# Performance work log

Hardware: AMD Instinct MI355X
Metric: run time of the kernel (lower is better)

Reference implementation:

```python
import jax, jax.numpy as jnp
import numpy as np

NUM_USERS = 100_000
NUM_JOBS = 100_000
N_NODES = NUM_USERS + NUM_JOBS
E = 3_200_000
D = 64  # embedding_dim == hidden_dim
B = 16_384


def setup_inputs() -> dict:
    key = jax.random.key(0)
    ks = jax.random.split(key, 10)
    edge_index = jax.random.randint(ks[0], (2, E), 0, N_NODES, dtype=jnp.int64)
    user_indices = jax.random.randint(ks[1], (B,), 0, NUM_USERS, dtype=jnp.int64)
    job_indices = jax.random.randint(ks[2], (B,), 0, NUM_JOBS, dtype=jnp.int64)
    # parameters (match reset_parameters: embeddings std=0.1, xavier pred, zero bias)
    user_emb_w = 0.1 * jax.random.normal(ks[3], (NUM_USERS, D), dtype=jnp.float32)
    job_emb_w = 0.1 * jax.random.normal(ks[4], (NUM_JOBS, D), dtype=jnp.float32)
    W1 = jax.random.normal(ks[5], (D, D), dtype=jnp.float32) / np.sqrt(D)
    b1 = jnp.zeros((D,), dtype=jnp.float32)
    W2 = jax.random.normal(ks[6], (D, D), dtype=jnp.float32) / np.sqrt(D)
    b2 = jnp.zeros((D,), dtype=jnp.float32)
    lim = np.sqrt(6.0 / (2 * D + 1))
    pred_w = jax.random.uniform(ks[7], (2 * D, 1), dtype=jnp.float32, minval=-lim, maxval=lim)
    pred_b = jnp.zeros((1,), dtype=jnp.float32)
    return {
        "edge_index": edge_index, "user_indices": user_indices, "job_indices": job_indices,
        "user_emb_w": user_emb_w, "job_emb_w": job_emb_w,
        "W1": W1, "b1": b1, "W2": W2, "b2": b2,
        "pred_w": pred_w, "pred_b": pred_b,
    }


def reference(edge_index, user_indices, job_indices, user_emb_w, job_emb_w, W1, b1, W2, b2, pred_w, pred_b):
    num_users = user_emb_w.shape[0]
    n = num_users + job_emb_w.shape[0]
    x = jnp.concatenate([user_emb_w, job_emb_w], axis=0)  # [N, D]

    # GCNConv (PyG defaults): add self-loops, symmetric D^-1/2 (A+I) D^-1/2 normalization
    loops = jnp.arange(n, dtype=edge_index.dtype)
    row = jnp.concatenate([edge_index[0], loops])  # source nodes
    col = jnp.concatenate([edge_index[1], loops])  # target nodes
    deg = jax.ops.segment_sum(jnp.ones_like(col, dtype=x.dtype), col, num_segments=n)
    dinv = jnp.where(deg > 0, jax.lax.rsqrt(jnp.maximum(deg, 1e-12)), 0.0)
    norm = dinv[row] * dinv[col]  # [E+N]

    def gcn_conv(h, W, b):
        h = h @ W                                   # [N, D]
        msg = h[row] * norm[:, None]                # gather + scale, [E+N, D]
        agg = jax.ops.segment_sum(msg, col, num_segments=n)  # scatter-add
        return agg + b

    x = jax.nn.relu(gcn_conv(x, W1, b1))  # dropout is identity at inference
    x = gcn_conv(x, W2, b2)

    user_emb = x[user_indices]                      # [B, D]
    job_emb = x[num_users + job_indices]            # [B, D]
    combined = jnp.concatenate([user_emb, job_emb], axis=1)  # [B, 2D]
    return (combined @ pred_w + pred_b)[:, 0]       # [B]
```

## Files before the change

kernel.cpp:

```cpp
#include <hip/hip_runtime.h>
#include <hip/hip_fp16.h>

#define D 64
#define BSHIFT 10
#define BMASK ((1 << BSHIFT) - 1)
#define NBUK_MAX 256
#define T_TILE 6144
#define EPT 24
#define CAP 20480

#if defined(__has_builtin)
#if __has_builtin(__builtin_amdgcn_fdot2)
#define HAVE_FDOT2 1
#endif
#endif

typedef _Float16 h2f __attribute__((ext_vector_type(2)));
typedef _Float16 half8v __attribute__((ext_vector_type(8)));
typedef float f4v __attribute__((ext_vector_type(4)));

__device__ __forceinline__ int wave_iscan(int v, int lane) {
#pragma unroll
    for (int off = 1; off < 64; off <<= 1) {
        int u = __shfl_up(v, off, 64);
        if (lane >= off) v += u;
    }
    return v;
}

__device__ __forceinline__ int block_escan(int v, int tid, int* wtot ) {
    int lane = tid & 63, w = tid >> 6;
    int inc = wave_iscan(v, lane);
    if (lane == 63) wtot[w] = inc;
    __syncthreads();
    int addv = 0;
#pragma unroll
    for (int q = 0; q < 4; q++) addv += (q < w) ? wtot[q] : 0;
    return inc - v + addv;
}

__device__ __forceinline__ float4 h4_to_f4(uint2 u) {
    __half2 a = *(__half2*)&u.x, b = *(__half2*)&u.y;
    float2 fa = __half22float2(a), fb = __half22float2(b);
    return make_float4(fa.x, fa.y, fb.x, fb.y);
}

__device__ __forceinline__ void acc_u2(float* acc, uint2 u) {
#ifdef HAVE_FDOT2
    h2f a0, a1;
    __builtin_memcpy(&a0, &u.x, 4);
    __builtin_memcpy(&a1, &u.y, 4);
    const h2f LO = {(_Float16)1.0f, (_Float16)0.0f};
    const h2f HI = {(_Float16)0.0f, (_Float16)1.0f};
    acc[0] = __builtin_amdgcn_fdot2(a0, LO, acc[0], false);
    acc[1] = __builtin_amdgcn_fdot2(a0, HI, acc[1], false);
    acc[2] = __builtin_amdgcn_fdot2(a1, LO, acc[2], false);
    acc[3] = __builtin_amdgcn_fdot2(a1, HI, acc[3], false);
#else
    float4 v = h4_to_f4(u);
    acc[0] += v.x; acc[1] += v.y; acc[2] += v.z; acc[3] += v.w;
#endif
}

__device__ __forceinline__ void acc_u4(float* acc, uint4 u) {
    uint2 a; a.x = u.x; a.y = u.y;
    uint2 b; b.x = u.z; b.y = u.w;
    acc_u2(acc, a);
    acc_u2(acc + 4, b);
}


__global__ __launch_bounds__(256) void k_bin(const int* __restrict__ row, const int* __restrict__ col,
                                             int E, int* __restrict__ bbase,
                                             unsigned* __restrict__ ebuf, int nbuk,
                                             const float* __restrict__ W1, const float* __restrict__ W2,
                                             __half* __restrict__ WT1, __half* __restrict__ WT2) {
    __shared__ int hist4[4][NBUK_MAX];
    __shared__ int sexcl[NBUK_MAX];
    __shared__ int cur4[4][NBUK_MAX];
    __shared__ int gbase[NBUK_MAX];
    __shared__ int wtot[4];
    __shared__ unsigned stage[T_TILE];
    __shared__ unsigned char sbuk[T_TILE];
    int tid = threadIdx.x;
    int w = tid >> 6;
    int tile0 = blockIdx.x * T_TILE;
    int cnt = min(T_TILE, E - tile0);

    if (blockIdx.x < 2) {
        const float* Ws = blockIdx.x ? W2 : W1;
        __half* Wd = blockIdx.x ? WT2 : WT1;
#pragma unroll
        for (int i = 0; i < 16; i++) {
            int f = i * 256 + tid;
            int k = f >> 6, c = f & 63;
            Wd[c * 64 + k] = __float2half(Ws[f]);
        }
    }

    unsigned pk[EPT];
    int bk[EPT];

#pragma unroll
    for (int q = 0; q < 4; q++) hist4[q][tid] = 0;
    __syncthreads();
#pragma unroll
    for (int j = 0; j < EPT; j++) {
        int i = tid + j * 256;
        if (i < cnt) {
            int r = row[tile0 + i];
            int c = col[tile0 + i];
            bk[j] = c >> BSHIFT;
            pk[j] = ((unsigned)(c & BMASK) << 18) | (unsigned)r;
            atomicAdd(&hist4[w][bk[j]], 1);
        } else {
            bk[j] = -1;
        }
    }
    __syncthreads();

    int h0 = hist4[0][tid], h1 = hist4[1][tid], h2 = hist4[2][tid], h3 = hist4[3][tid];
    int v = h0 + h1 + h2 + h3;
    int excl = block_escan(v, tid, wtot);
    sexcl[tid] = excl;
    cur4[0][tid] = excl;
    cur4[1][tid] = excl + h0;
    cur4[2][tid] = excl + h0 + h1;
    cur4[3][tid] = excl + h0 + h1 + h2;
    gbase[tid] = (v > 0 && tid < nbuk) ? (tid * CAP + atomicAdd(&bbase[tid], v)) : 0;
    __syncthreads();

#pragma unroll
    for (int j = 0; j < EPT; j++) {
        if (bk[j] >= 0) {
            int p = atomicAdd(&cur4[w][bk[j]], 1);
            stage[p] = pk[j];
            sbuk[p] = (unsigned char)bk[j];
        }
    }
    __syncthreads();

    for (int i = tid; i < cnt; i += 256) {
        int b = sbuk[i];
        int gpos = gbase[b] + (i - sexcl[b]);
        ebuf[gpos] = stage[i];
    }
}


__global__ __launch_bounds__(256) void k_csr2a(const unsigned* __restrict__ ebuf,
                                               const int* __restrict__ bbase, int N,
                                               int2* __restrict__ rps, float* __restrict__ dinv,
                                               __half* __restrict__ h) {
    __shared__ int lcnt[1 << BSHIFT];
    __shared__ int wtot[4];
    int tid = threadIdx.x;
    int c0 = blockIdx.x << BSHIFT;
    int nn = min(1 << BSHIFT, N - c0);
    int e0 = blockIdx.x * CAP, e1 = e0 + bbase[blockIdx.x];

    if (blockIdx.x == 0 && tid < 16) {
        uint2 z; z.x = 0u; z.y = 0u;
        *(uint2*)(h + (size_t)N * D + tid * 4) = z;
    }

    for (int i = tid; i < (1 << BSHIFT); i += 256) lcnt[i] = 0;
    __syncthreads();
    for (int j = e0 + tid; j < e1; j += 256)
        atomicAdd(&lcnt[ebuf[j] >> 18], 1);
    __syncthreads();

    int c[4]; int s = 0;
#pragma unroll
    for (int i = 0; i < 4; i++) { c[i] = lcnt[tid * 4 + i]; s += c[i]; }
    int run = block_escan(s, tid, wtot);
#pragma unroll
    for (int i = 0; i < 4; i++) {
        int idx = tid * 4 + i;
        if (idx < nn) {
            int st = e0 + run;
            rps[c0 + idx] = make_int2(st, st + c[i]);
            dinv[c0 + idx] = rsqrtf((float)(c[i] + 1));
        }
        run += c[i];
    }
}


__device__ __forceinline__ void stage_Wt(const __half* __restrict__ WTg, __half* __restrict__ Wt, int tid) {
#pragma unroll
    for (int i = 0; i < 2; i++) {
        int f = (i * 256 + tid) * 8;
        int c = f >> 6, k = f & 63;
        *(half8v*)(Wt + c * 72 + k) = *(const half8v*)(WTg + f);
    }
}

__device__ __forceinline__ void gemm_compute(const __half* __restrict__ Xh, const __half* __restrict__ Wt,
                                             int n0, int N, const float* __restrict__ dinvp,
                                             __half* __restrict__ out, int tid) {
    int lane = tid & 63;
    int wv = tid >> 6;
    int n16 = lane & 15, quad = lane >> 4;
    const __half* Xw = Xh + (wv * 16) * 72;
    half8v a0 = *(const half8v*)(Xw + n16 * 72 + quad * 8);
    half8v a1 = *(const half8v*)(Xw + n16 * 72 + quad * 8 + 32);
    f4v acc[4];
#pragma unroll
    for (int ct = 0; ct < 4; ct++) {
        acc[ct] = (f4v){0.f, 0.f, 0.f, 0.f};
        const __half* wp = Wt + (ct * 16 + n16) * 72;
        half8v b0 = *(const half8v*)(wp + quad * 8);
        half8v b1 = *(const half8v*)(wp + quad * 8 + 32);
        acc[ct] = __builtin_amdgcn_mfma_f32_16x16x32_f16(a0, b0, acc[ct], 0, 0, 0);
        acc[ct] = __builtin_amdgcn_mfma_f32_16x16x32_f16(a1, b1, acc[ct], 0, 0, 0);
    }
#pragma unroll
    for (int r = 0; r < 4; r++) {
        int node = n0 + wv * 16 + quad * 4 + r;
        if (node < N) {
            float dv = dinvp[node];
#pragma unroll
            for (int ct = 0; ct < 4; ct++)
                out[(size_t)node * D + ct * 16 + n16] = __float2half(acc[ct][r] * dv);
        }
    }
}


__global__ __launch_bounds__(256) void k_csr2b_gemm1(const unsigned* __restrict__ ebuf,
                                                     const int2* __restrict__ rps,
                                                     const int* __restrict__ bbase,
                                                     int N, int nbuk, int* __restrict__ srcs,
                                                     const float* __restrict__ xu, const float* __restrict__ xj,
                                                     int U, const __half* __restrict__ WT1,
                                                     const float* __restrict__ dinv, __half* __restrict__ h) {
    __shared__ __align__(16) __half Xh[64 * 72];
    __shared__ __align__(16) __half Wt[64 * 72];
    int tid = threadIdx.x;
    if ((int)blockIdx.x < nbuk) {
        int* lcur = (int*)Xh;
        int c0 = blockIdx.x << BSHIFT;
        int e0 = blockIdx.x * CAP, e1 = e0 + bbase[blockIdx.x];
        for (int i = tid; i < (1 << BSHIFT); i += 256)
            lcur[i] = (c0 + i < N) ? rps[c0 + i].x : 0;
        __syncthreads();
        for (int j = e0 + tid; j < e1; j += 256) {
            unsigned pk = ebuf[j];
            int p = atomicAdd(&lcur[pk >> 18], 1);
            srcs[p] = (int)(pk & 0x3ffffu);
        }
    } else {
        int n0 = ((int)blockIdx.x - nbuk) * 64;
        stage_Wt(WT1, Wt, tid);
#pragma unroll
        for (int i = 0; i < 4; i++) {
            int e4 = i * 256 + tid;
            int nl = e4 >> 4, k4 = e4 & 15;
            int nn = n0 + nl;
            uint2 st; st.x = 0u; st.y = 0u;
            if (nn < N) {
                const float* src = (nn < U) ? (xu + (size_t)nn * D) : (xj + (size_t)(nn - U) * D);
                float4 v = *(const float4*)(src + k4 * 4);
                __half2 p0 = __floats2half2_rn(v.x, v.y);
                __half2 p1 = __floats2half2_rn(v.z, v.w);
                st.x = *(unsigned*)&p0; st.y = *(unsigned*)&p1;
            }
            *(uint2*)(Xh + nl * 72 + k4 * 4) = st;
        }
        __syncthreads();
        gemm_compute(Xh, Wt, n0, N, dinv, h, tid);
    }
}


__device__ __forceinline__ void gather8(float* acc, const __half* __restrict__ hs,
                                        const int2* __restrict__ rps,
                                        const int* __restrict__ srcs,
                                        int node, int N, int g, int t) {
    const __half* hp = hs + t * 8;
    int2 r = rps[node];
    int e0 = r.x, deg = r.y - r.x;
    for (int cb = 0; cb < deg; cb += 8) {
        int sv = (cb + t < deg) ? srcs[e0 + cb + t] : N;
        int base = g * 8;
        int s0 = __shfl(sv, base + 0, 64);
        int s1 = __shfl(sv, base + 1, 64);
        int s2 = __shfl(sv, base + 2, 64);
        int s3 = __shfl(sv, base + 3, 64);
        int s4 = __shfl(sv, base + 4, 64);
        int s5 = __shfl(sv, base + 5, 64);
        int s6 = __shfl(sv, base + 6, 64);
        int s7 = __shfl(sv, base + 7, 64);
        uint4 u0 = *(const uint4*)(hp + (size_t)s0 * D);
        uint4 u1 = *(const uint4*)(hp + (size_t)s1 * D);
        uint4 u2 = *(const uint4*)(hp + (size_t)s2 * D);
        uint4 u3 = *(const uint4*)(hp + (size_t)s3 * D);
        uint4 u4 = *(const uint4*)(hp + (size_t)s4 * D);
        uint4 u5 = *(const uint4*)(hp + (size_t)s5 * D);
        uint4 u6 = *(const uint4*)(hp + (size_t)s6 * D);
        uint4 u7 = *(const uint4*)(hp + (size_t)s7 * D);
        acc_u4(acc, u0);
        acc_u4(acc, u1);
        acc_u4(acc, u2);
        acc_u4(acc, u3);
        acc_u4(acc, u4);
        acc_u4(acc, u5);
        acc_u4(acc, u6);
        acc_u4(acc, u7);
    }
}


__global__ __launch_bounds__(256) void k_agg_gemm2(const __half* __restrict__ hs, const float* __restrict__ dinv,
                                                   const int2* __restrict__ rps, const int* __restrict__ srcs,
                                                   const float* __restrict__ bias, const __half* __restrict__ WT2,
                                                   const float* __restrict__ pw, int N,
                                                   float* __restrict__ zu, float* __restrict__ zj) {
    __shared__ __align__(16) __half Xh[64 * 72];
    __shared__ __align__(16) __half Wt[64 * 72];
    int tid = threadIdx.x;
    int lane = tid & 63;
    int w = tid >> 6;
    int g = lane >> 3, t = lane & 7;
    int n0 = blockIdx.x * 64;

    stage_Wt(WT2, Wt, tid);

    float4 ba = *(const float4*)(bias + t * 8);
    float4 bb = *(const float4*)(bias + t * 8 + 4);
#pragma unroll
    for (int rr = 0; rr < 2; rr++) {
        int nl = w * 16 + rr * 8 + g;
        int node = n0 + nl;
        uint4 st; st.x = 0u; st.y = 0u; st.z = 0u; st.w = 0u;
        if (node < N) {
            float acc[8] = {0.f, 0.f, 0.f, 0.f, 0.f, 0.f, 0.f, 0.f};
            gather8(acc, hs, rps, srcs, node, N, g, t);
            uint4 su = *(const uint4*)(hs + (size_t)node * D + t * 8);
            float4 sa = h4_to_f4(make_uint2(su.x, su.y));
            float4 sb = h4_to_f4(make_uint2(su.z, su.w));
            float dv = dinv[node];
            float o0 = fmaxf((acc[0] + sa.x) * dv + ba.x, 0.f);
            float o1 = fmaxf((acc[1] + sa.y) * dv + ba.y, 0.f);
            float o2 = fmaxf((acc[2] + sa.z) * dv + ba.z, 0.f);
            float o3 = fmaxf((acc[3] + sa.w) * dv + ba.w, 0.f);
            float o4 = fmaxf((acc[4] + sb.x) * dv + bb.x, 0.f);
            float o5 = fmaxf((acc[5] + sb.y) * dv + bb.y, 0.f);
            float o6 = fmaxf((acc[6] + sb.z) * dv + bb.z, 0.f);
            float o7 = fmaxf((acc[7] + sb.w) * dv + bb.w, 0.f);
            __half2 p0 = __floats2half2_rn(o0, o1);
            __half2 p1 = __floats2half2_rn(o2, o3);
            __half2 p2 = __floats2half2_rn(o4, o5);
            __half2 p3 = __floats2half2_rn(o6, o7);
            st.x = *(unsigned*)&p0; st.y = *(unsigned*)&p1;
            st.z = *(unsigned*)&p2; st.w = *(unsigned*)&p3;
        }
        *(uint4*)(Xh + nl * 72 + t * 8) = st;
    }
    __syncthreads();

    int wv = w;
    int n16 = lane & 15, quad = lane >> 4;
    const __half* Xw = Xh + (wv * 16) * 72;
    half8v a0 = *(const half8v*)(Xw + n16 * 72 + quad * 8);
    half8v a1 = *(const half8v*)(Xw + n16 * 72 + quad * 8 + 32);
    f4v acc[4];
    float pwu_r[4], pwj_r[4];
#pragma unroll
    for (int ct = 0; ct < 4; ct++) {
        pwu_r[ct] = pw[ct * 16 + n16];
        pwj_r[ct] = pw[64 + ct * 16 + n16];
        acc[ct] = (f4v){0.f, 0.f, 0.f, 0.f};
        const __half* wp = Wt + (ct * 16 + n16) * 72;
        half8v b0 = *(const half8v*)(wp + quad * 8);
        half8v b1 = *(const half8v*)(wp + quad * 8 + 32);
        acc[ct] = __builtin_amdgcn_mfma_f32_16x16x32_f16(a0, b0, acc[ct], 0, 0, 0);
        acc[ct] = __builtin_amdgcn_mfma_f32_16x16x32_f16(a1, b1, acc[ct], 0, 0, 0);
    }
#pragma unroll
    for (int r = 0; r < 4; r++) {
        int node = n0 + wv * 16 + quad * 4 + r;
        float dv = (node < N) ? dinv[node] : 0.0f;
        float su = acc[0][r] * pwu_r[0] + acc[1][r] * pwu_r[1]
                 + acc[2][r] * pwu_r[2] + acc[3][r] * pwu_r[3];
        float sj = acc[0][r] * pwj_r[0] + acc[1][r] * pwj_r[1]
                 + acc[2][r] * pwj_r[2] + acc[3][r] * pwj_r[3];
        su += __shfl_xor(su, 1, 64); sj += __shfl_xor(sj, 1, 64);
        su += __shfl_xor(su, 2, 64); sj += __shfl_xor(sj, 2, 64);
        su += __shfl_xor(su, 4, 64); sj += __shfl_xor(sj, 4, 64);
        su += __shfl_xor(su, 8, 64); sj += __shfl_xor(sj, 8, 64);
        if (n16 == 0 && node < N) {
            zu[node] = su * dv;
            zj[node] = sj * dv;
        }
    }
}


__global__ __launch_bounds__(256) void k_pred(const float* __restrict__ zu, const float* __restrict__ zj,
                                              const float* __restrict__ dinv,
                                              const int2* __restrict__ rps, const int* __restrict__ srcs,
                                              const float* __restrict__ b2, const float* __restrict__ pw,
                                              const float* __restrict__ pb,
                                              const int* __restrict__ uidx, const int* __restrict__ jidx,
                                              int U, int N, int B, float* __restrict__ out) {
    int tid = threadIdx.x;
    int lane = tid & 63;
    int g = lane >> 3, t = lane & 7;
    int pair = blockIdx.x * 16 + (tid >> 6) * 4 + (g >> 1);
    if (pair >= B) return;
    int side = g & 1;
    int c = side ? (U + jidx[pair]) : uidx[pair];
    const float* zt = side ? zj : zu;

    float4 b2a = *(const float4*)(b2 + t * 8);
    float4 b2b = *(const float4*)(b2 + t * 8 + 4);
    float4 wa = *(const float4*)(pw + side * 64 + t * 8);
    float4 wb = *(const float4*)(pw + side * 64 + t * 8 + 4);
    float cpart = b2a.x * wa.x + b2a.y * wa.y + b2a.z * wa.z + b2a.w * wa.w
                + b2b.x * wb.x + b2b.y * wb.y + b2b.z * wb.z + b2b.w * wb.w;

    int2 r = rps[c];
    int deg = r.y - r.x;
    float s = 0.f;
    for (int cb = 0; cb < deg; cb += 8) {
        if (cb + t < deg) s += zt[srcs[r.x + cb + t]];
    }
    s += __shfl_xor(s, 1, 64); cpart += __shfl_xor(cpart, 1, 64);
    s += __shfl_xor(s, 2, 64); cpart += __shfl_xor(cpart, 2, 64);
    s += __shfl_xor(s, 4, 64); cpart += __shfl_xor(cpart, 4, 64);

    float val = (s + zt[c]) * dinv[c] + cpart;
    val += __shfl_xor(val, 8, 64);
    if ((lane & 15) == 0) out[pair] = val + pb[0];
}


extern "C" void kernel_launch(void* const* d_in, const int* in_sizes, int n_in,
                              void* d_out, int out_size, void* d_ws, size_t ws_size,
                              hipStream_t stream) {
    const int*   edge = (const int*)d_in[0];
    const int*   uidx = (const int*)d_in[1];
    const int*   jidx = (const int*)d_in[2];
    const float* xu   = (const float*)d_in[3];
    const float* xj   = (const float*)d_in[4];
    const float* W1   = (const float*)d_in[5];
    const float* b1   = (const float*)d_in[6];
    const float* W2   = (const float*)d_in[7];
    const float* b2   = (const float*)d_in[8];
    const float* pw   = (const float*)d_in[9];
    const float* pb   = (const float*)d_in[10];
    float* out = (float*)d_out;

    int E = in_sizes[0] / 2;
    int B = in_sizes[1];
    int U = in_sizes[3] / D;
    int J = in_sizes[4] / D;
    int N = U + J;
    int nbuk = (N + (1 << BSHIFT) - 1) >> BSHIFT;
    const int* row = edge;
    const int* col = edge + E;

    char* p = (char*)d_ws;
    auto alloc = [&](size_t bytes) -> void* {
        void* q = (void*)p;
        p += (bytes + 255) / 256 * 256;
        return q;
    };
    size_t capsz = (size_t)nbuk * CAP * 4;
    int*      bbase = (int*)alloc(256 * 4);
    int2*     rps   = (int2*)alloc((size_t)N * 8);
    float*    dinv  = (float*)alloc((size_t)N * 4);
    int*      srcs  = (int*)alloc(capsz);
    __half*   h     = (__half*)alloc((size_t)(N + 1) * D * 2);
    unsigned* ebuf  = (unsigned*)alloc(capsz);
    float*    zu    = (float*)alloc((size_t)N * 4);
    float*    zj    = (float*)alloc((size_t)N * 4);
    __half*   WT1   = (__half*)alloc((size_t)D * D * 2);
    __half*   WT2   = (__half*)alloc((size_t)D * D * 2);

    hipMemsetAsync(bbase, 0, 256 * 4, stream);

    k_bin<<<(E + T_TILE - 1) / T_TILE, 256, 0, stream>>>(row, col, E, bbase, ebuf, nbuk,
                                                         W1, W2, WT1, WT2);

    k_csr2a<<<nbuk, 256, 0, stream>>>(ebuf, bbase, N, rps, dinv, h);

    k_csr2b_gemm1<<<nbuk + (N + 63) / 64, 256, 0, stream>>>(ebuf, rps, bbase, N, nbuk, srcs,
                                                            xu, xj, U, WT1, dinv, h);

    k_agg_gemm2<<<(N + 63) / 64, 256, 0, stream>>>(h, dinv, rps, srcs, b1, WT2, pw, N, zu, zj);

    k_pred<<<(B + 15) / 16, 256, 0, stream>>>(zu, zj, dinv, rps, srcs, b2, pw, pb,
                                              uidx, jidx, U, N, B, out);
}
```

Measured before the change: 259.0 us.

## Vectorize edge loads, move fp16 conversion to CSR pass, widen neighbor gather

The edge-binning kernel now reads row and column indices as int4 vectors, and the CSR count and fill passes read packed edges as uint4. The fp32 to fp16 embedding conversion moves into extra blocks of the CSR-count kernel, which write h. The GEMM1 blocks then read fp16 h and overwrite it in place with the transformed rows. The aggregation gather handles 16 neighbors per iteration instead of 8 to keep more loads in flight, at the cost of extra registers and an added fp16 write and read pass over h.

Result: faster. 242.4 us (-6.4%).

```diff
diff --git a/kernel.cpp b/kernel.cpp
--- a/kernel.cpp
+++ b/kernel.cpp
@@ -105,16 +105,35 @@
     for (int q = 0; q < 4; q++) hist4[q][tid] = 0;
     __syncthreads();
 #pragma unroll
-    for (int j = 0; j < EPT; j++) {
-        int i = tid + j * 256;
-        if (i < cnt) {
-            int r = row[tile0 + i];
-            int c = col[tile0 + i];
-            bk[j] = c >> BSHIFT;
-            pk[j] = ((unsigned)(c & BMASK) << 18) | (unsigned)r;
-            atomicAdd(&hist4[w][bk[j]], 1);
+    for (int j = 0; j < EPT / 4; j++) {
+        int i4 = j * 1024 + tid * 4;
+        if (i4 + 3 < cnt) {
+            int4 r4 = *(const int4*)(row + tile0 + i4);
+            int4 c4 = *(const int4*)(col + tile0 + i4);
+            int rr[4] = {r4.x, r4.y, r4.z, r4.w};
+            int cc[4] = {c4.x, c4.y, c4.z, c4.w};
+#pragma unroll
+            for (int q = 0; q < 4; q++) {
+                int jj = j * 4 + q;
+                bk[jj] = cc[q] >> BSHIFT;
+                pk[jj] = ((unsigned)(cc[q] & BMASK) << 18) | (unsigned)rr[q];
+                atomicAdd(&hist4[w][bk[jj]], 1);
+            }
         } else {
-            bk[j] = -1;
+#pragma unroll
+            for (int q = 0; q < 4; q++) {
+                int jj = j * 4 + q;
+                int i = i4 + q;
+                if (i < cnt) {
+                    int r = row[tile0 + i];
+                    int c = col[tile0 + i];
+                    bk[jj] = c >> BSHIFT;
+                    pk[jj] = ((unsigned)(c & BMASK) << 18) | (unsigned)r;
+                    atomicAdd(&hist4[w][bk[jj]], 1);
+                } else {
+                    bk[jj] = -1;
+                }
+            }
         }
     }
     __syncthreads();
@@ -148,13 +167,39 @@
 }
 
 
-__global__ __launch_bounds__(256) void k_csr2a(const unsigned* __restrict__ ebuf,
-                                               const int* __restrict__ bbase, int N,
-                                               int2* __restrict__ rps, float* __restrict__ dinv,
-                                               __half* __restrict__ h) {
+__global__ __launch_bounds__(256) void k_csr2a_conv(const unsigned* __restrict__ ebuf,
+                                                    const int* __restrict__ bbase, int N, int nbuk,
+                                                    int2* __restrict__ rps, float* __restrict__ dinv,
+                                                    const float* __restrict__ xu, const float* __restrict__ xj,
+                                                    int U, __half* __restrict__ h) {
     __shared__ int lcnt[1 << BSHIFT];
     __shared__ int wtot[4];
     int tid = threadIdx.x;
+
+    if ((int)blockIdx.x >= nbuk) {
+        int m0 = ((int)blockIdx.x - nbuk) * 128;
+#pragma unroll
+        for (int i = 0; i < 4; i++) {
+            int slot = i * 256 + tid;
+            int nl = slot >> 3, q = slot & 7;
+            int nn = m0 + nl;
+            if (nn < N) {
+                const float* src = (nn < U) ? (xu + (size_t)nn * D) : (xj + (size_t)(nn - U) * D);
+                float4 a = *(const float4*)(src + q * 8);
+                float4 b = *(const float4*)(src + q * 8 + 4);
+                __half2 p0 = __floats2half2_rn(a.x, a.y);
+                __half2 p1 = __floats2half2_rn(a.z, a.w);
+                __half2 p2 = __floats2half2_rn(b.x, b.y);
+                __half2 p3 = __floats2half2_rn(b.z, b.w);
+                uint4 st;
+                st.x = *(unsigned*)&p0; st.y = *(unsigned*)&p1;
+                st.z = *(unsigned*)&p2; st.w = *(unsigned*)&p3;
+                *(uint4*)(h + (size_t)nn * D + q * 8) = st;
+            }
+        }
+        return;
+    }
+
     int c0 = blockIdx.x << BSHIFT;
     int nn = min(1 << BSHIFT, N - c0);
     int e0 = blockIdx.x * CAP, e1 = e0 + bbase[blockIdx.x];
@@ -166,8 +211,16 @@
 
     for (int i = tid; i < (1 << BSHIFT); i += 256) lcnt[i] = 0;
     __syncthreads();
-    for (int j = e0 + tid; j < e1; j += 256)
-        atomicAdd(&lcnt[ebuf[j] >> 18], 1);
+    int len = e1 - e0;
+    int nf = len & ~3;
+    for (int j = tid * 4; j < nf; j += 1024) {
+        uint4 v = *(const uint4*)(ebuf + e0 + j);
+        atomicAdd(&lcnt[v.x >> 18], 1);
+        atomicAdd(&lcnt[v.y >> 18], 1);
+        atomicAdd(&lcnt[v.z >> 18], 1);
+        atomicAdd(&lcnt[v.w >> 18], 1);
+    }
+    if (tid < (len - nf)) atomicAdd(&lcnt[ebuf[e0 + nf + tid] >> 18], 1);
     __syncthreads();
 
     int c[4]; int s = 0;
@@ -186,7 +239,6 @@
     }
 }
 
-
 __device__ __forceinline__ void stage_Wt(const __half* __restrict__ WTg, __half* __restrict__ Wt, int tid) {
 #pragma unroll
     for (int i = 0; i < 2; i++) {
@@ -196,44 +248,12 @@
     }
 }
 
-__device__ __forceinline__ void gemm_compute(const __half* __restrict__ Xh, const __half* __restrict__ Wt,
-                                             int n0, int N, const float* __restrict__ dinvp,
-                                             __half* __restrict__ out, int tid) {
-    int lane = tid & 63;
-    int wv = tid >> 6;
-    int n16 = lane & 15, quad = lane >> 4;
-    const __half* Xw = Xh + (wv * 16) * 72;
-    half8v a0 = *(const half8v*)(Xw + n16 * 72 + quad * 8);
-    half8v a1 = *(const half8v*)(Xw + n16 * 72 + quad * 8 + 32);
-    f4v acc[4];
-#pragma unroll
-    for (int ct = 0; ct < 4; ct++) {
-        acc[ct] = (f4v){0.f, 0.f, 0.f, 0.f};
-        const __half* wp = Wt + (ct * 16 + n16) * 72;
-        half8v b0 = *(const half8v*)(wp + quad * 8);
-        half8v b1 = *(const half8v*)(wp + quad * 8 + 32);
-        acc[ct] = __builtin_amdgcn_mfma_f32_16x16x32_f16(a0, b0, acc[ct], 0, 0, 0);
-        acc[ct] = __builtin_amdgcn_mfma_f32_16x16x32_f16(a1, b1, acc[ct], 0, 0, 0);
-    }
-#pragma unroll
-    for (int r = 0; r < 4; r++) {
-        int node = n0 + wv * 16 + quad * 4 + r;
-        if (node < N) {
-            float dv = dinvp[node];
-#pragma unroll
-            for (int ct = 0; ct < 4; ct++)
-                out[(size_t)node * D + ct * 16 + n16] = __float2half(acc[ct][r] * dv);
-        }
-    }
-}
-
 
 __global__ __launch_bounds__(256) void k_csr2b_gemm1(const unsigned* __restrict__ ebuf,
                                                      const int2* __restrict__ rps,
                                                      const int* __restrict__ bbase,
                                                      int N, int nbuk, int* __restrict__ srcs,
-                                                     const float* __restrict__ xu, const float* __restrict__ xj,
-                                                     int U, const __half* __restrict__ WT1,
+                                                     const __half* __restrict__ WT1,
                                                      const float* __restrict__ dinv, __half* __restrict__ h) {
     __shared__ __align__(16) __half Xh[64 * 72];
     __shared__ __align__(16) __half Wt[64 * 72];
@@ -245,8 +265,17 @@
         for (int i = tid; i < (1 << BSHIFT); i += 256)
             lcur[i] = (c0 + i < N) ? rps[c0 + i].x : 0;
         __syncthreads();
-        for (int j = e0 + tid; j < e1; j += 256) {
-            unsigned pk = ebuf[j];
+        int len = e1 - e0;
+        int nf = len & ~3;
+        for (int j = tid * 4; j < nf; j += 1024) {
+            uint4 v = *(const uint4*)(ebuf + e0 + j);
+            int p0 = atomicAdd(&lcur[v.x >> 18], 1); srcs[p0] = (int)(v.x & 0x3ffffu);
+            int p1 = atomicAdd(&lcur[v.y >> 18], 1); srcs[p1] = (int)(v.y & 0x3ffffu);
+            int p2 = atomicAdd(&lcur[v.z >> 18], 1); srcs[p2] = (int)(v.z & 0x3ffffu);
+            int p3 = atomicAdd(&lcur[v.w >> 18], 1); srcs[p3] = (int)(v.w & 0x3ffffu);
+        }
+        if (tid < (len - nf)) {
+            unsigned pk = ebuf[e0 + nf + tid];
             int p = atomicAdd(&lcur[pk >> 18], 1);
             srcs[p] = (int)(pk & 0x3ffffu);
         }
@@ -254,60 +283,71 @@
         int n0 = ((int)blockIdx.x - nbuk) * 64;
         stage_Wt(WT1, Wt, tid);
 #pragma unroll
-        for (int i = 0; i < 4; i++) {
-            int e4 = i * 256 + tid;
-            int nl = e4 >> 4, k4 = e4 & 15;
+        for (int i = 0; i < 2; i++) {
+            int slot = i * 256 + tid;
+            int nl = slot >> 3, q = slot & 7;
             int nn = n0 + nl;
-            uint2 st; st.x = 0u; st.y = 0u;
-            if (nn < N) {
-                const float* src = (nn < U) ? (xu + (size_t)nn * D) : (xj + (size_t)(nn - U) * D);
-                float4 v = *(const float4*)(src + k4 * 4);
-                __half2 p0 = __floats2half2_rn(v.x, v.y);
-                __half2 p1 = __floats2half2_rn(v.z, v.w);
-                st.x = *(unsigned*)&p0; st.y = *(unsigned*)&p1;
+            uint4 st; st.x = 0u; st.y = 0u; st.z = 0u; st.w = 0u;
+            if (nn < N) st = *(const uint4*)(h + (size_t)nn * D + q * 8);
+            *(uint4*)(Xh + nl * 72 + q * 8) = st;
+        }
+        __syncthreads();
+
+        int lane = tid & 63;
+        int wv = tid >> 6;
+        int n16 = lane & 15, quad = lane >> 4;
+        const __half* Xw = Xh + (wv * 16) * 72;
+        half8v a0 = *(const half8v*)(Xw + n16 * 72 + quad * 8);
+        half8v a1 = *(const half8v*)(Xw + n16 * 72 + quad * 8 + 32);
+        f4v acc[4];
+#pragma unroll
+        for (int ct = 0; ct < 4; ct++) {
+            acc[ct] = (f4v){0.f, 0.f, 0.f, 0.f};
+            const __half* wp = Wt + (ct * 16 + n16) * 72;
+            half8v b0 = *(const half8v*)(wp + quad * 8);
+            half8v b1 = *(const half8v*)(wp + quad * 8 + 32);
+            acc[ct] = __builtin_amdgcn_mfma_f32_16x16x32_f16(a0, b0, acc[ct], 0, 0, 0);
+            acc[ct] = __builtin_amdgcn_mfma_f32_16x16x32_f16(a1, b1, acc[ct], 0, 0, 0);
+        }
+#pragma unroll
+        for (int r = 0; r < 4; r++) {
+            int node = n0 + wv * 16 + quad * 4 + r;
+            if (node < N) {
+                float dv = dinv[node];
+#pragma unroll
+                for (int ct = 0; ct < 4; ct++)
+                    h[(size_t)node * D + ct * 16 + n16] = __float2half(acc[ct][r] * dv);
             }
-            *(uint2*)(Xh + nl * 72 + k4 * 4) = st;
-        }
-        __syncthreads();
-        gemm_compute(Xh, Wt, n0, N, dinv, h, tid);
-    }
-}
-
-
-__device__ __forceinline__ void gather8(float* acc, const __half* __restrict__ hs,
-                                        const int2* __restrict__ rps,
-                                        const int* __restrict__ srcs,
-                                        int node, int N, int g, int t) {
+        }
+    }
+}
+
+
+__device__ __forceinline__ void gather16(float* acc, const __half* __restrict__ hs,
+                                         const int2* __restrict__ rps,
+                                         const int* __restrict__ srcs,
+                                         int node, int N, int g, int t) {
     const __half* hp = hs + t * 8;
     int2 r = rps[node];
     int e0 = r.x, deg = r.y - r.x;
-    for (int cb = 0; cb < deg; cb += 8) {
-        int sv = (cb + t < deg) ? srcs[e0 + cb + t] : N;
-        int base = g * 8;
-        int s0 = __shfl(sv, base + 0, 64);
-        int s1 = __shfl(sv, base + 1, 64);
-        int s2 = __shfl(sv, base + 2, 64);
-        int s3 = __shfl(sv, base + 3, 64);
-        int s4 = __shfl(sv, base + 4, 64);
-        int s5 = __shfl(sv, base + 5, 64);
-        int s6 = __shfl(sv, base + 6, 64);
-        int s7 = __shfl(sv, base + 7, 64);
-        uint4 u0 = *(const uint4*)(hp + (size_t)s0 * D);
-        uint4 u1 = *(const uint4*)(hp + (size_t)s1 * D);
-        uint4 u2 = *(const uint4*)(hp + (size_t)s2 * D);
-        uint4 u3 = *(const uint4*)(hp + (size_t)s3 * D);
-        uint4 u4 = *(const uint4*)(hp + (size_t)s4 * D);
-        uint4 u5 = *(const uint4*)(hp + (size_t)s5 * D);
-        uint4 u6 = *(const uint4*)(hp + (size_t)s6 * D);
-        uint4 u7 = *(const uint4*)(hp + (size_t)s7 * D);
-        acc_u4(acc, u0);
-        acc_u4(acc, u1);
-        acc_u4(acc, u2);
-        acc_u4(acc, u3);
-        acc_u4(acc, u4);
-        acc_u4(acc, u5);
-        acc_u4(acc, u6);
-        acc_u4(acc, u7);
+    int base = g * 8;
+    for (int cb = 0; cb < deg; cb += 16) {
+        int svA = (cb + t < deg) ? srcs[e0 + cb + t] : N;
+        int svB = (cb + 8 + t < deg) ? srcs[e0 + cb + 8 + t] : N;
+        int sA[8], sB[8];
+#pragma unroll
+        for (int q = 0; q < 8; q++) sA[q] = __shfl(svA, base + q, 64);
+#pragma unroll
+        for (int q = 0; q < 8; q++) sB[q] = __shfl(svB, base + q, 64);
+        uint4 uA[8], uB[8];
+#pragma unroll
+        for (int q = 0; q < 8; q++) uA[q] = *(const uint4*)(hp + (size_t)sA[q] * D);
+#pragma unroll
+        for (int q = 0; q < 8; q++) uB[q] = *(const uint4*)(hp + (size_t)sB[q] * D);
+#pragma unroll
+        for (int q = 0; q < 8; q++) acc_u4(acc, uA[q]);
+#pragma unroll
+        for (int q = 0; q < 8; q++) acc_u4(acc, uB[q]);
     }
 }
 
@@ -336,7 +376,7 @@
         uint4 st; st.x = 0u; st.y = 0u; st.z = 0u; st.w = 0u;
         if (node < N) {
             float acc[8] = {0.f, 0.f, 0.f, 0.f, 0.f, 0.f, 0.f, 0.f};
-            gather8(acc, hs, rps, srcs, node, N, g, t);
+            gather16(acc, hs, rps, srcs, node, N, g, t);
             uint4 su = *(const uint4*)(hs + (size_t)node * D + t * 8);
             float4 sa = h4_to_f4(make_uint2(su.x, su.y));
             float4 sb = h4_to_f4(make_uint2(su.z, su.w));
@@ -459,6 +499,7 @@
     int J = in_sizes[4] / D;
     int N = U + J;
     int nbuk = (N + (1 << BSHIFT) - 1) >> BSHIFT;
+    int nconv = (N + 127) / 128;
     const int* row = edge;
     const int* col = edge + E;
 
@@ -485,10 +526,11 @@
     k_bin<<<(E + T_TILE - 1) / T_TILE, 256, 0, stream>>>(row, col, E, bbase, ebuf, nbuk,
                                                          W1, W2, WT1, WT2);
 
-    k_csr2a<<<nbuk, 256, 0, stream>>>(ebuf, bbase, N, rps, dinv, h);
+    k_csr2a_conv<<<nbuk + nconv, 256, 0, stream>>>(ebuf, bbase, N, nbuk, rps, dinv,
+                                                   xu, xj, U, h);
 
     k_csr2b_gemm1<<<nbuk + (N + 63) / 64, 256, 0, stream>>>(ebuf, rps, bbase, N, nbuk, srcs,
-                                                            xu, xj, U, WT1, dinv, h);
+                                                            WT1, dinv, h);
 
     k_agg_gemm2<<<(N + 63) / 64, 256, 0, stream>>>(h, dinv, rps, srcs, b1, WT2, pw, N, zu, zj);
 
```
